# Optimization experiments

Hardware: AMD Instinct MI355X
Metric: run time of the kernel (lower is better)

## Reference

```python
import jax, jax.numpy as jnp
import numpy as np

A_BIT = 4
W_BIT = 4
EPS = 1e-5

# representative 3x3 binary kernel patterns (pattern_dic entries)
_PAT1 = np.array([[0, 1, 0], [1, 1, 1], [0, 1, 0]], dtype=np.float32)
_PAT2 = np.array([[1, 0, 1], [0, 1, 0], [1, 0, 1]], dtype=np.float32)


def _ste_round(x):
    return x + jax.lax.stop_gradient(jnp.round(x) - x)


def _quantize_k(x, k):
    n = float(2 ** k - 1)
    return _ste_round(x * n) / n


def _act_quant(x, a_bit=A_BIT):
    # Activate: ReLU then clamp to [0,1] and k-bit uniform quantize (DoReFa)
    return _quantize_k(jnp.clip(x, 0.0, 1.0), a_bit)


def _weight_quant(w, w_bit=W_BIT):
    # DoReFa weight quantization: tanh / max|tanh| -> [0,1] -> k-bit -> [-1,1]
    t = jnp.tanh(w)
    t = t / (2.0 * jnp.max(jnp.abs(t))) + 0.5
    return 2.0 * _quantize_k(t, w_bit) - 1.0


def _bn(x, gamma, beta):
    # training-mode BN over (N,H,W)
    m = jnp.mean(x, axis=(0, 2, 3), keepdims=True)
    v = jnp.var(x, axis=(0, 2, 3), keepdims=True)
    xhat = (x - m) * jax.lax.rsqrt(v + EPS)
    return xhat * gamma[None, :, None, None] + beta[None, :, None, None]


def _conv3x3(x, w):
    # NCHW x OIHW, stride 1, padding 1
    return jax.lax.conv_general_dilated(
        x, w, window_strides=(1, 1), padding=((1, 1), (1, 1)),
        dimension_numbers=('NCHW', 'OIHW', 'NCHW'))


def setup_inputs() -> dict:
    key = jax.random.key(0)
    k1, k2, k3 = jax.random.split(key, 3)
    B, C, H, W = 128, 128, 16, 16
    fan = C * 9
    return {
        'x': jax.random.normal(k1, (B, C, H, W), dtype=jnp.float32),
        'gamma1': jnp.ones((C,), jnp.float32),
        'beta1': jnp.zeros((C,), jnp.float32),
        'gamma2': jnp.ones((C,), jnp.float32),
        'beta2': jnp.zeros((C,), jnp.float32),
        'w1': jax.random.normal(k2, (C, C, 3, 3), jnp.float32) / np.sqrt(fan),
        'w2': jax.random.normal(k3, (C, C, 3, 3), jnp.float32) / np.sqrt(fan),
        'pat1': jnp.asarray(_PAT1),
        'pat2': jnp.asarray(_PAT2),
    }


def reference(x, gamma1, beta1, gamma2, beta2, w1, w2, pat1, pat2):
    # conv1(act1(bn1(x))) with pattern-masked quantized weights
    h = _act_quant(_bn(x, gamma1, beta1))
    wq1 = _weight_quant(w1) * pat1[None, None, :, :]
    out = _conv3x3(h, wq1)
    # dropout is identity in eval mode
    out = _act_quant(_bn(out, gamma2, beta2))
    wq2 = _weight_quant(w2) * pat2[None, None, :, :]
    out = _conv3x3(out, wq2)
    # identity shortcut (in_planes == planes, stride == 1)
    return out + x
```

## Files before the change

kernel.cpp:

```cpp
#include <hip/hip_runtime.h>
#include <math.h>

#define BATCH 128
#define CHN   128
#define HW    256
#define PLANE (CHN*HW)
#define WELEM (CHN*CHN*9)

using int4v  = __attribute__((ext_vector_type(4))) int;
using int16v = __attribute__((ext_vector_type(16))) int;
typedef unsigned int u32;

__device__ __forceinline__ void gload16(const void* g, void* l) {
    __builtin_amdgcn_global_load_lds((const __attribute__((address_space(1))) u32*)g,
                                     (__attribute__((address_space(3))) u32*)l, 16, 0, 0);
}


__device__ __forceinline__ float wave_sum(float v) {
    #pragma unroll
    for (int off = 32; off; off >>= 1) v += __shfl_down(v, off, 64);
    return v;
}
__device__ __forceinline__ float wave_max(float v) {
    #pragma unroll
    for (int off = 32; off; off >>= 1) v = fmaxf(v, __shfl_down(v, off, 64));
    return v;
}

extern "C" __global__ void __launch_bounds__(256)
k_pre1(const float* __restrict__ x,
       const float* __restrict__ w1, const float* __restrict__ w2,
       float* __restrict__ s1part, float* __restrict__ wmaxp) {
    int b = blockIdx.x;
    int t = threadIdx.x;
    int lane = t & 63, wid = t >> 6;
    __shared__ float ls[8];

    if (b < 512) {
        int c = b >> 2, q = b & 3;
        const float* p = x + (size_t)(q * 32) * PLANE + c * HW + t;
        float s = 0.f, s2 = 0.f;
        #pragma unroll 8
        for (int n = 0; n < 32; ++n) {
            float v = p[n * PLANE];
            s += v; s2 += v * v;
        }
        s = wave_sum(s); s2 = wave_sum(s2);
        if (lane == 0) { ls[wid] = s; ls[4 + wid] = s2; }
        __syncthreads();
        if (t == 0) {
            s1part[b * 2]     = ls[0] + ls[1] + ls[2] + ls[3];
            s1part[b * 2 + 1] = ls[4] + ls[5] + ls[6] + ls[7];
        }
    } else {
        int i2 = b - 512;
        int y = (i2 >= 72) ? 1 : 0;
        int blk = i2 - y * 72;
        const float* w = y ? w2 : w1;
        int i = blk * 2048 + t;
        float m = 0.f;
        #pragma unroll
        for (int k = 0; k < 8; ++k)
            m = fmaxf(m, fabsf(tanhf(w[i + k * 256])));
        m = wave_max(m);
        if (lane == 0) ls[wid] = m;
        __syncthreads();
        if (t == 0)
            wmaxp[y * 72 + blk] = fmaxf(fmaxf(ls[0], ls[1]), fmaxf(ls[2], ls[3]));
    }
}

extern "C" __global__ void __launch_bounds__(256)
k_mid(const float* __restrict__ x,
      const float* __restrict__ w1, const float* __restrict__ w2,
      const float* __restrict__ pat1, const float* __restrict__ pat2,
      const float* __restrict__ gamma1, const float* __restrict__ beta1,
      const float* __restrict__ s1part, const float* __restrict__ wmaxp,
      unsigned long long* __restrict__ gS, unsigned long long* __restrict__ gQ,
      signed char* __restrict__ wq1, signed char* __restrict__ wq2,
      unsigned char* __restrict__ hbufT) {
    int b = blockIdx.x;
    int t = threadIdx.x;

    if (b < 256) {
        __shared__ u32 tmp[32 * 129];
        __shared__ float2 tab[128];
        int n = b >> 1, half = b & 1;
        if (t < 128) {
            float S  = s1part[(4 * t) * 2]     + s1part[(4 * t + 1) * 2]
                     + s1part[(4 * t + 2) * 2] + s1part[(4 * t + 3) * 2];
            float S2 = s1part[(4 * t) * 2 + 1] + s1part[(4 * t + 1) * 2 + 1]
                     + s1part[(4 * t + 2) * 2 + 1] + s1part[(4 * t + 3) * 2 + 1];
            float mean = S * (1.f / 32768.f);
            float var  = S2 * (1.f / 32768.f) - mean * mean;
            float istd = 1.0f / sqrtf(var + 1e-5f);
            float sc = istd * gamma1[t];
            float sh = beta1[t] - mean * sc;
            tab[t] = make_float2(sc, sh);
        }
        __syncthreads();

        const float* sp = x + (size_t)n * PLANE + half * 128;
        #pragma unroll 8
        for (int j = 0; j < 16; ++j) {
            int id = j * 256 + t;
            int cch = id >> 5, p4 = id & 31;
            float sc = tab[cch].x, sh = tab[cch].y;
            float4 v = *(const float4*)(sp + cch * HW + p4 * 4);
            unsigned q0 = (unsigned)(int)rintf(fminf(fmaxf(v.x * sc + sh, 0.f), 1.f) * 15.f);
            unsigned q1 = (unsigned)(int)rintf(fminf(fmaxf(v.y * sc + sh, 0.f), 1.f) * 15.f);
            unsigned q2 = (unsigned)(int)rintf(fminf(fmaxf(v.z * sc + sh, 0.f), 1.f) * 15.f);
            unsigned q3 = (unsigned)(int)rintf(fminf(fmaxf(v.w * sc + sh, 0.f), 1.f) * 15.f);
            tmp[p4 * 129 + cch] = q0 | (q1 << 8) | (q2 << 16) | (q3 << 24);
        }
        __syncthreads();

        unsigned char* dp = hbufT + (size_t)n * PLANE + half * 128 * CHN;
        int p4 = t >> 3;
        int c0 = (t & 7) * 16;
        u32 w[16];
        #pragma unroll
        for (int k = 0; k < 16; ++k) w[k] = tmp[p4 * 129 + c0 + k];
        #pragma unroll
        for (int pp = 0; pp < 4; ++pp) {
            int p = p4 * 4 + pp;
            int pg = half * 128 + p;
            int r = ((pg >> 4) + 1) * 18 + (pg & 15) + 1;
            int xr = (r & 7) << 4;
            int s = pp * 8;
            int4v o;
            o.x = (int)(((w[0] >> s) & 255u) | (((w[1] >> s) & 255u) << 8) |
                        (((w[2] >> s) & 255u) << 16) | (((w[3] >> s) & 255u) << 24));
            o.y = (int)(((w[4] >> s) & 255u) | (((w[5] >> s) & 255u) << 8) |
                        (((w[6] >> s) & 255u) << 16) | (((w[7] >> s) & 255u) << 24));
            o.z = (int)(((w[8] >> s) & 255u) | (((w[9] >> s) & 255u) << 8) |
                        (((w[10] >> s) & 255u) << 16) | (((w[11] >> s) & 255u) << 24));
            o.w = (int)(((w[12] >> s) & 255u) | (((w[13] >> s) & 255u) << 8) |
                        (((w[14] >> s) & 255u) << 16) | (((w[15] >> s) & 255u) << 24));
            *(int4v*)(dp + p * 128 + (c0 ^ xr)) = o;
        }
    } else {
        int i2 = b - 256;
        int y  = (i2 >= 577) ? 1 : 0;
        int xb = i2 - y * 577;

        if (xb == 576) {
            if (y == 0) {
                for (int k = t; k < 1024; k += 256) { gS[k] = 0ull; gQ[k] = 0ull; }
            }
            return;
        }
        const float* w   = y ? w2 : w1;
        const float* pat = y ? pat2 : pat1;
        signed char* wq  = y ? wq2 : wq1;

        __shared__ float lm[72];
        if (t < 72) lm[t] = wmaxp[y * 72 + t];
        __syncthreads();
        float M = lm[0];
        #pragma unroll
        for (int k = 1; k < 72; ++k) M = fmaxf(M, lm[k]);

        int i = xb * 256 + t;
        int j = i & 15;
        int c = i >> 4;
        int ocq = c / 2304;
        int rem = c - ocq * 2304;
        int tap = rem >> 8;
        int r2  = rem & 255;
        int q   = r2 >> 6;
        int hq  = (r2 >> 5) & 1;
        int l31 = r2 & 31;
        int oc = ocq * 32 + l31;
        int ic = q * 32 + hq * 16 + j;
        float tv = tanhf(w[(oc * CHN + ic) * 9 + tap]);
        float tn = tv / (2.0f * M) + 0.5f;
        int mq = (int)rintf(tn * 15.f);
        mq = mq < 0 ? 0 : (mq > 15 ? 15 : mq);
        int qv = 2 * mq - 15;
        if (pat[tap] == 0.f) qv = 0;
        wq[i] = (signed char)qv;
    }
}

__device__ __forceinline__ void zero_halo(unsigned char* A, int t) {
    int4v z; z.x = 0; z.y = 0; z.z = 0; z.w = 0;
    for (int cidx = t; cidx < 544; cidx += 256) {
        int hrow = cidx >> 3, ch = cidx & 7;
        int r;
        if (hrow < 18) r = hrow;
        else if (hrow < 36) r = 306 + (hrow - 18);
        else { int h2 = hrow - 36; r = (1 + (h2 & 15)) * 18 + ((h2 >> 4) ? 17 : 0); }
        *(int4v*)(A + r * 128 + ch * 16) = z;
    }
}
__device__ __forceinline__ void stage_act(const unsigned char* ap, unsigned char* A,
                                          int wid, int lane) {
    #pragma unroll
    for (int j = 0; j < 8; ++j) {
        int p0w = j * 32 + wid * 8;
        int r0 = ((p0w >> 4) + 1) * 18 + (p0w & 15) + 1;
        gload16(ap + p0w * 128 + (lane << 4), A + r0 * 128);
    }
}
__device__ __forceinline__ void stage_W(const unsigned char* wsrc, unsigned char* W,
                                        int wid, int lane) {
    #pragma unroll
    for (int it = 0; it < 9; ++it)
        gload16(wsrc + it * 4096 + wid * 1024 + (lane << 4),
                W + it * 4096 + wid * 1024);
}
__device__ __forceinline__ void mfma_full(const unsigned char* A, const unsigned char* W,
                                          const bool pf[9],
                                          int h0, int w0c, int h1, int w1c,
                                          int cbase, int lane,
                                          int16v& acc0, int16v& acc1) {
    #pragma unroll
    for (int tap = 0; tap < 9; ++tap) {
        if (pf[tap]) {
            int dy = tap / 3, dx = tap % 3;
            int r0 = (h0 + dy) * 18 + (w0c + dx);
            int r1 = (h1 + dy) * 18 + (w1c + dx);
            int b0base = r0 * 128 + (cbase ^ ((r0 & 7) << 4));
            int b1base = r1 * 128 + (cbase ^ ((r1 & 7) << 4));
            const unsigned char* wt = W + tap * 4096 + (lane << 4);
            #pragma unroll
            for (int q = 0; q < 4; ++q) {
                int4v a0 = *(const int4v*)(wt + q * 1024);
                int4v b0 = *(const int4v*)(A + (b0base ^ (q << 5)));
                int4v b1 = *(const int4v*)(A + (b1base ^ (q << 5)));
                acc0 = __builtin_amdgcn_mfma_i32_32x32x32_i8(a0, b0, acc0, 0, 0, 0);
                acc1 = __builtin_amdgcn_mfma_i32_32x32x32_i8(a0, b1, acc1, 0, 0, 0);
            }
        }
    }
}

extern "C" __global__ void __launch_bounds__(256, 2)
k_conv1s(const unsigned char* __restrict__ actT,
         const signed char*  __restrict__ wq,
         const float* __restrict__ pat,
         unsigned long long* __restrict__ gS, unsigned long long* __restrict__ gQ) {
    int n = blockIdx.x, ocq = blockIdx.y;
    int t = threadIdx.x;
    int lane = t & 63, wid = t >> 6;
    int l31 = lane & 31, hq = lane >> 5;

    __shared__ __align__(16) unsigned char lds[41472 + 36864];
    unsigned char* A = lds;
    unsigned char* W = lds + 41472;

    zero_halo(A, t);
    stage_W((const unsigned char*)wq + (size_t)ocq * 36864, W, wid, lane);
    stage_act(actT + (size_t)n * PLANE, A, wid, lane);

    bool pf[9];
    #pragma unroll
    for (int j = 0; j < 9; ++j) pf[j] = (pat[j] != 0.f);

    __syncthreads();

    int16v acc0, acc1;
    #pragma unroll
    for (int e = 0; e < 16; ++e) { acc0[e] = 0; acc1[e] = 0; }

    int p0 = wid * 64 + l31;
    int h0 = p0 >> 4, w0c = p0 & 15;
    int p1 = p0 + 32;
    int h1 = p1 >> 4, w1c = p1 & 15;
    int cbase = hq * 16;

    mfma_full(A, W, pf, h0, w0c, h1, w1c, cbase, lane, acc0, acc1);

    __syncthreads();
    int*       lsm = (int*)lds;
    long long* lq  = (long long*)(lds + 512);
    #pragma unroll
    for (int e = 0; e < 16; ++e) {
        int a0 = acc0[e], a1 = acc1[e];
        int s = a0 + a1;
        long long qq = (long long)a0 * a0 + (long long)a1 * a1;
        #pragma unroll
        for (int off = 1; off < 32; off <<= 1) {
            s  += __shfl_xor(s, off, 64);
            qq += __shfl_xor(qq, off, 64);
        }
        if (l31 == 0) {
            int ch = (e & 3) + 8 * (e >> 2) + 4 * hq;
            lsm[wid * 32 + ch] = s;
            lq [wid * 32 + ch] = qq;
        }
    }
    __syncthreads();
    if (t < 32) {
        long long S = 0, Q = 0;
        #pragma unroll
        for (int w = 0; w < 4; ++w) { S += lsm[w * 32 + t]; Q += lq[w * 32 + t]; }
        int sh = (n & 7) * 128 + ocq * 32 + t;
        atomicAdd(gS + sh, (unsigned long long)S);
        atomicAdd(gQ + sh, (unsigned long long)Q);
    }
}

extern "C" __global__ void __launch_bounds__(256, 2)
k_conv2(const unsigned char* __restrict__ hb,
        const signed char* __restrict__ wq1, const signed char* __restrict__ wq2,
        const float* __restrict__ pat1, const float* __restrict__ pat2,
        const float* __restrict__ gamma2, const float* __restrict__ beta2,
        const unsigned long long* __restrict__ gS, const unsigned long long* __restrict__ gQ,
        const float* __restrict__ x, float* __restrict__ out) {
    int n = blockIdx.x, ocq = blockIdx.y;
    int t = threadIdx.x;
    int lane = t & 63, wid = t >> 6;
    int l31 = lane & 31, hq = lane >> 5;

    __shared__ __align__(16) unsigned char lds[41472 + 36864];
    __shared__ float2 tab[128];
    unsigned char* A = lds;
    unsigned char* W = lds + 41472;

    if (t < 128) {
        long long S = 0, Q = 0;
        #pragma unroll
        for (int r = 0; r < 8; ++r) {
            S += (long long)gS[r * 128 + t];
            Q += (long long)gQ[r * 128 + t];
        }
        double mean = (double)S * (1.0 / (32768.0 * 225.0));
        double ex2  = (double)Q * (1.0 / (32768.0 * 225.0 * 225.0));
        double var  = ex2 - mean * mean;
        float istd = (float)(1.0 / sqrt(var + 1e-5));
        float sc = istd * gamma2[t];
        float sh = beta2[t] - (float)mean * sc;
        tab[t] = make_float2(sc, sh);
    }

    zero_halo(A, t);
    stage_act(hb + (size_t)n * PLANE, A, wid, lane);

    bool pf1[9], pf2[9];
    #pragma unroll
    for (int j = 0; j < 9; ++j) { pf1[j] = (pat1[j] != 0.f); pf2[j] = (pat2[j] != 0.f); }

    int p0 = wid * 64 + l31;
    int h0 = p0 >> 4, w0c = p0 & 15;
    int p1 = p0 + 32;
    int h1 = p1 >> 4, w1c = p1 & 15;
    int cbase = hq * 16;

    int4v cod[4][2];
    int16v acc0, acc1;

    #pragma unroll
    for (int tt = 0; tt < 4; ++tt) {
        stage_W((const unsigned char*)wq1 + (size_t)tt * 36864, W, wid, lane);
        __syncthreads();

        #pragma unroll
        for (int e = 0; e < 16; ++e) { acc0[e] = 0; acc1[e] = 0; }
        mfma_full(A, W, pf1, h0, w0c, h1, w1c, cbase, lane, acc0, acc1);

        #pragma unroll
        for (int h2 = 0; h2 < 2; ++h2) {
            const int16v& ac = h2 ? acc1 : acc0;
            u32 wrd[4];
            #pragma unroll
            for (int k = 0; k < 4; ++k) {
                u32 pk = 0;
                #pragma unroll
                for (int e2 = 0; e2 < 4; ++e2) {
                    int e = 4 * k + e2;
                    int row = (e & 3) + 8 * k + 4 * hq;
                    float2 ss = tab[tt * 32 + row];
                    float v = (float)ac[e] * (1.f / 225.f);
                    u32 q = (u32)(int)rintf(fminf(fmaxf(v * ss.x + ss.y, 0.f), 1.f) * 15.f);
                    pk |= q << (8 * e2);
                }
                wrd[k] = pk;
            }
            u32 prt[4];
            #pragma unroll
            for (int k = 0; k < 4; ++k) prt[k] = __shfl_xor(wrd[k], 32, 64);
            int4v o;
            if (hq == 0) { o.x = (int)wrd[0]; o.y = (int)prt[0]; o.z = (int)wrd[1]; o.w = (int)prt[1]; }
            else         { o.x = (int)prt[2]; o.y = (int)wrd[2]; o.z = (int)prt[3]; o.w = (int)wrd[3]; }
            cod[tt][h2] = o;
        }
        __syncthreads();
    }

    #pragma unroll
    for (int tt = 0; tt < 4; ++tt) {
        #pragma unroll
        for (int h2 = 0; h2 < 2; ++h2) {
            int p = h2 ? p1 : p0;
            int c0 = tt * 32 + (hq ? 16 : 0);
            int r = ((p >> 4) + 1) * 18 + (p & 15) + 1;
            int xr = (r & 7) << 4;
            *(int4v*)(A + r * 128 + (c0 ^ xr)) = cod[tt][h2];
        }
    }
    stage_W((const unsigned char*)wq2 + (size_t)ocq * 36864, W, wid, lane);
    __syncthreads();

    #pragma unroll
    for (int e = 0; e < 16; ++e) { acc0[e] = 0; acc1[e] = 0; }
    mfma_full(A, W, pf2, h0, w0c, h1, w1c, cbase, lane, acc0, acc1);

    float* ob = out + ((size_t)n * CHN + ocq * 32) * HW;
    const float* xb = x + ((size_t)n * CHN + ocq * 32) * HW;
    #pragma unroll
    for (int e = 0; e < 16; ++e) {
        int row = (e & 3) + 8 * (e >> 2) + 4 * hq;
        int idx0 = row * HW + wid * 64 + l31;
        ob[idx0]      = (float)acc0[e] * (1.f / 225.f) + xb[idx0];
        ob[idx0 + 32] = (float)acc1[e] * (1.f / 225.f) + xb[idx0 + 32];
    }
}

extern "C" void kernel_launch(void* const* d_in, const int* in_sizes, int n_in,
                              void* d_out, int out_size, void* d_ws, size_t ws_size,
                              hipStream_t stream) {
    const float* x      = (const float*)d_in[0];
    const float* gamma1 = (const float*)d_in[1];
    const float* beta1  = (const float*)d_in[2];
    const float* gamma2 = (const float*)d_in[3];
    const float* beta2  = (const float*)d_in[4];
    const float* w1     = (const float*)d_in[5];
    const float* w2     = (const float*)d_in[6];
    const float* pat1   = (const float*)d_in[7];
    const float* pat2   = (const float*)d_in[8];
    float* out = (float*)d_out;

    char* ws = (char*)d_ws;
    float* wmaxp     = (float*)(ws + 0);
    float* s1part    = (float*)(ws + 2048);
    unsigned long long* gS = (unsigned long long*)(ws + 6144);
    unsigned long long* gQ = (unsigned long long*)(ws + 14336);
    signed char* wq1 = (signed char*)(ws + 22528);
    signed char* wq2 = (signed char*)(ws + 169984);
    unsigned char* hbufT = (unsigned char*)(ws + 317440);

    k_pre1<<<656, 256, 0, stream>>>(x, w1, w2, s1part, wmaxp);
    k_mid<<<256 + 2 * 577, 256, 0, stream>>>(x, w1, w2, pat1, pat2, gamma1, beta1,
                                             s1part, wmaxp, gS, gQ, wq1, wq2, hbufT);
    k_conv1s<<<dim3(BATCH, 4), 256, 0, stream>>>(hbufT, wq1, pat1, gS, gQ);
    k_conv2<<<dim3(BATCH, 4), 256, 0, stream>>>(hbufT, wq1, wq2, pat1, pat2,
                                                gamma2, beta2, gS, gQ, x, out);
}
```

Measured before the change: 45.91 us.

## Split second-stage conv into separate act2 kernel to stop redundant conv1 recompute

Previously every k_conv2 block recomputed the full first convolution for all four output-channel quarters, then re-quantized the result into LDS before running the second convolution. A new k_act2 kernel now computes only its own quarter of conv1, applies BN2 and 4-bit quantization, and writes the packed activations to a new global workspace buffer. k_conv2 then just stages that buffer and wq2 and runs a single MFMA pass. This removes about four times redundant conv1 MFMA work. In exchange it adds an extra kernel launch and a global write and read of the intermediate activations.

```diff
diff --git a/kernel.cpp b/kernel.cpp
--- a/kernel.cpp
+++ b/kernel.cpp
@@ -304,11 +304,97 @@
 }
 
 extern "C" __global__ void __launch_bounds__(256, 2)
-k_conv2(const unsigned char* __restrict__ hb,
-        const signed char* __restrict__ wq1, const signed char* __restrict__ wq2,
-        const float* __restrict__ pat1, const float* __restrict__ pat2,
-        const float* __restrict__ gamma2, const float* __restrict__ beta2,
-        const unsigned long long* __restrict__ gS, const unsigned long long* __restrict__ gQ,
+k_act2(const unsigned char* __restrict__ hb,
+       const signed char* __restrict__ wq1,
+       const float* __restrict__ pat1,
+       const float* __restrict__ gamma2, const float* __restrict__ beta2,
+       const unsigned long long* __restrict__ gS, const unsigned long long* __restrict__ gQ,
+       unsigned char* __restrict__ hb2) {
+    int n = blockIdx.x, ocq = blockIdx.y;
+    int t = threadIdx.x;
+    int lane = t & 63, wid = t >> 6;
+    int l31 = lane & 31, hq = lane >> 5;
+
+    __shared__ __align__(16) unsigned char lds[41472 + 36864];
+    __shared__ float2 tab[32];
+    unsigned char* A = lds;
+    unsigned char* W = lds + 41472;
+
+    if (t < 32) {
+        int ch = ocq * 32 + t;
+        long long S = 0, Q = 0;
+        #pragma unroll
+        for (int r = 0; r < 8; ++r) {
+            S += (long long)gS[r * 128 + ch];
+            Q += (long long)gQ[r * 128 + ch];
+        }
+        double mean = (double)S * (1.0 / (32768.0 * 225.0));
+        double ex2  = (double)Q * (1.0 / (32768.0 * 225.0 * 225.0));
+        double var  = ex2 - mean * mean;
+        float istd = (float)(1.0 / sqrt(var + 1e-5));
+        float sc = istd * gamma2[ch];
+        float sh = beta2[ch] - (float)mean * sc;
+        tab[t] = make_float2(sc, sh);
+    }
+
+    zero_halo(A, t);
+    stage_W((const unsigned char*)wq1 + (size_t)ocq * 36864, W, wid, lane);
+    stage_act(hb + (size_t)n * PLANE, A, wid, lane);
+
+    bool pf[9];
+    #pragma unroll
+    for (int j = 0; j < 9; ++j) pf[j] = (pat1[j] != 0.f);
+
+    __syncthreads();
+
+    int16v acc0, acc1;
+    #pragma unroll
+    for (int e = 0; e < 16; ++e) { acc0[e] = 0; acc1[e] = 0; }
+
+    int p0 = wid * 64 + l31;
+    int h0 = p0 >> 4, w0c = p0 & 15;
+    int p1 = p0 + 32;
+    int h1 = p1 >> 4, w1c = p1 & 15;
+    int cbase = hq * 16;
+
+    mfma_full(A, W, pf, h0, w0c, h1, w1c, cbase, lane, acc0, acc1);
+
+    #pragma unroll
+    for (int h2 = 0; h2 < 2; ++h2) {
+        const int16v& ac = h2 ? acc1 : acc0;
+        int p = h2 ? p1 : p0;
+        u32 wrd[4];
+        #pragma unroll
+        for (int k = 0; k < 4; ++k) {
+            u32 pk = 0;
+            #pragma unroll
+            for (int e2 = 0; e2 < 4; ++e2) {
+                int e = 4 * k + e2;
+                int row = (e & 3) + 8 * k + 4 * hq;
+                float2 ss = tab[row];
+                float v = (float)ac[e] * (1.f / 225.f);
+                u32 q = (u32)(int)rintf(fminf(fmaxf(v * ss.x + ss.y, 0.f), 1.f) * 15.f);
+                pk |= q << (8 * e2);
+            }
+            wrd[k] = pk;
+        }
+        u32 prt[4];
+        #pragma unroll
+        for (int k = 0; k < 4; ++k) prt[k] = __shfl_xor(wrd[k], 32, 64);
+        int4v o;
+        if (hq == 0) { o.x = (int)wrd[0]; o.y = (int)prt[0]; o.z = (int)wrd[1]; o.w = (int)prt[1]; }
+        else         { o.x = (int)prt[2]; o.y = (int)wrd[2]; o.z = (int)prt[3]; o.w = (int)wrd[3]; }
+        int c0 = ocq * 32 + (hq ? 16 : 0);
+        int r = ((p >> 4) + 1) * 18 + (p & 15) + 1;
+        int xr = (r & 7) << 4;
+        *(int4v*)(hb2 + (size_t)n * PLANE + p * 128 + (c0 ^ xr)) = o;
+    }
+}
+
+extern "C" __global__ void __launch_bounds__(256, 2)
+k_conv2(const unsigned char* __restrict__ hb2,
+        const signed char* __restrict__ wq2,
+        const float* __restrict__ pat2,
         const float* __restrict__ x, float* __restrict__ out) {
     int n = blockIdx.x, ocq = blockIdx.y;
     int t = threadIdx.x;
@@ -316,32 +402,22 @@
     int l31 = lane & 31, hq = lane >> 5;
 
     __shared__ __align__(16) unsigned char lds[41472 + 36864];
-    __shared__ float2 tab[128];
     unsigned char* A = lds;
     unsigned char* W = lds + 41472;
 
-    if (t < 128) {
-        long long S = 0, Q = 0;
-        #pragma unroll
-        for (int r = 0; r < 8; ++r) {
-            S += (long long)gS[r * 128 + t];
-            Q += (long long)gQ[r * 128 + t];
-        }
-        double mean = (double)S * (1.0 / (32768.0 * 225.0));
-        double ex2  = (double)Q * (1.0 / (32768.0 * 225.0 * 225.0));
-        double var  = ex2 - mean * mean;
-        float istd = (float)(1.0 / sqrt(var + 1e-5));
-        float sc = istd * gamma2[t];
-        float sh = beta2[t] - (float)mean * sc;
-        tab[t] = make_float2(sc, sh);
-    }
-
     zero_halo(A, t);
-    stage_act(hb + (size_t)n * PLANE, A, wid, lane);
-
-    bool pf1[9], pf2[9];
-    #pragma unroll
-    for (int j = 0; j < 9; ++j) { pf1[j] = (pat1[j] != 0.f); pf2[j] = (pat2[j] != 0.f); }
+    stage_W((const unsigned char*)wq2 + (size_t)ocq * 36864, W, wid, lane);
+    stage_act(hb2 + (size_t)n * PLANE, A, wid, lane);
+
+    bool pf[9];
+    #pragma unroll
+    for (int j = 0; j < 9; ++j) pf[j] = (pat2[j] != 0.f);
+
+    __syncthreads();
+
+    int16v acc0, acc1;
+    #pragma unroll
+    for (int e = 0; e < 16; ++e) { acc0[e] = 0; acc1[e] = 0; }
 
     int p0 = wid * 64 + l31;
     int h0 = p0 >> 4, w0c = p0 & 15;
@@ -349,64 +425,7 @@
     int h1 = p1 >> 4, w1c = p1 & 15;
     int cbase = hq * 16;
 
-    int4v cod[4][2];
-    int16v acc0, acc1;
-
-    #pragma unroll
-    for (int tt = 0; tt < 4; ++tt) {
-        stage_W((const unsigned char*)wq1 + (size_t)tt * 36864, W, wid, lane);
-        __syncthreads();
-
-        #pragma unroll
-        for (int e = 0; e < 16; ++e) { acc0[e] = 0; acc1[e] = 0; }
-        mfma_full(A, W, pf1, h0, w0c, h1, w1c, cbase, lane, acc0, acc1);
-
-        #pragma unroll
-        for (int h2 = 0; h2 < 2; ++h2) {
-            const int16v& ac = h2 ? acc1 : acc0;
-            u32 wrd[4];
-            #pragma unroll
-            for (int k = 0; k < 4; ++k) {
-                u32 pk = 0;
-                #pragma unroll
-                for (int e2 = 0; e2 < 4; ++e2) {
-                    int e = 4 * k + e2;
-                    int row = (e & 3) + 8 * k + 4 * hq;
-                    float2 ss = tab[tt * 32 + row];
-                    float v = (float)ac[e] * (1.f / 225.f);
-                    u32 q = (u32)(int)rintf(fminf(fmaxf(v * ss.x + ss.y, 0.f), 1.f) * 15.f);
-                    pk |= q << (8 * e2);
-                }
-                wrd[k] = pk;
-            }
-            u32 prt[4];
-            #pragma unroll
-            for (int k = 0; k < 4; ++k) prt[k] = __shfl_xor(wrd[k], 32, 64);
-            int4v o;
-            if (hq == 0) { o.x = (int)wrd[0]; o.y = (int)prt[0]; o.z = (int)wrd[1]; o.w = (int)prt[1]; }
-            else         { o.x = (int)prt[2]; o.y = (int)wrd[2]; o.z = (int)prt[3]; o.w = (int)wrd[3]; }
-            cod[tt][h2] = o;
-        }
-        __syncthreads();
-    }
-
-    #pragma unroll
-    for (int tt = 0; tt < 4; ++tt) {
-        #pragma unroll
-        for (int h2 = 0; h2 < 2; ++h2) {
-            int p = h2 ? p1 : p0;
-            int c0 = tt * 32 + (hq ? 16 : 0);
-            int r = ((p >> 4) + 1) * 18 + (p & 15) + 1;
-            int xr = (r & 7) << 4;
-            *(int4v*)(A + r * 128 + (c0 ^ xr)) = cod[tt][h2];
-        }
-    }
-    stage_W((const unsigned char*)wq2 + (size_t)ocq * 36864, W, wid, lane);
-    __syncthreads();
-
-    #pragma unroll
-    for (int e = 0; e < 16; ++e) { acc0[e] = 0; acc1[e] = 0; }
-    mfma_full(A, W, pf2, h0, w0c, h1, w1c, cbase, lane, acc0, acc1);
+    mfma_full(A, W, pf, h0, w0c, h1, w1c, cbase, lane, acc0, acc1);
 
     float* ob = out + ((size_t)n * CHN + ocq * 32) * HW;
     const float* xb = x + ((size_t)n * CHN + ocq * 32) * HW;
@@ -441,11 +460,12 @@
     signed char* wq1 = (signed char*)(ws + 22528);
     signed char* wq2 = (signed char*)(ws + 169984);
     unsigned char* hbufT = (unsigned char*)(ws + 317440);
+    unsigned char* hbuf2 = (unsigned char*)(ws + 4511744);
 
     k_pre1<<<656, 256, 0, stream>>>(x, w1, w2, s1part, wmaxp);
     k_mid<<<256 + 2 * 577, 256, 0, stream>>>(x, w1, w2, pat1, pat2, gamma1, beta1,
                                              s1part, wmaxp, gS, gQ, wq1, wq2, hbufT);
     k_conv1s<<<dim3(BATCH, 4), 256, 0, stream>>>(hbufT, wq1, pat1, gS, gQ);
-    k_conv2<<<dim3(BATCH, 4), 256, 0, stream>>>(hbufT, wq1, wq2, pat1, pat2,
-                                                gamma2, beta2, gS, gQ, x, out);
-}
+    k_act2<<<dim3(BATCH, 4), 256, 0, stream>>>(hbufT, wq1, pat1, gamma2, beta2, gS, gQ, hbuf2);
+    k_conv2<<<dim3(BATCH, 4), 256, 0, stream>>>(hbuf2, wq2, pat2, x, out);
+}
```

Measured after the change: 41.74 us. 1.1x faster.
